# Optimization experiments

Measured on AMD Instinct MI355X. Metric: run time of the kernel, lower is better.

Reference implementation:

```python
import jax, jax.numpy as jnp
import numpy as np


def setup_inputs() -> dict:
    key = jax.random.key(0)
    k1, k2, k3 = jax.random.split(key, 3)
    B, S, E = 4, 8192, 1024
    x = jax.random.normal(k1, (B, S, E), dtype=jnp.float32)
    # torch nn.Linear weights have shape [out_features, in_features]
    W1 = jax.random.normal(k2, (3 * E, E), dtype=jnp.float32) * (1.0 / np.sqrt(E))
    W2 = jax.random.normal(k3, (E, E), dtype=jnp.float32) * (1.0 / np.sqrt(E))
    return {"x": x, "W1": W1, "W2": W2, "heads": 16}


def reference(x, W1, W2, heads):
    B, S, E = x.shape
    h = heads
    e = E // h
    # qkv projection: [B,S,3E] -> 'b s (n h e) -> n b h s e'
    qkv = (x @ W1.T).reshape(B, S, 3, h, e)
    qkv = jnp.transpose(qkv, (2, 0, 3, 1, 4))  # [3,B,h,S,e]
    q, k, v = qkv[0], qkv[1], qkv[2]
    # score: [B,h,e,e], softmax over last dim (c)
    score = jax.nn.softmax(jnp.einsum('bhnk,bhnc->bhkc', k / 4, v), axis=-1)
    # einsum 'bhnk,bhkc->bhnk': elementwise over k, sum over c
    attn = jax.nn.softmax(jnp.einsum('bhnk,bhkc->bhnk', q / 4, score), axis=-1)
    # 'b h s e -> b s (h e)' then linear_2
    out = jnp.transpose(attn, (0, 2, 1, 3)).reshape(B, S, E) @ W2.T
    return out
```

## Files before the change

kernel.cpp:

```cpp
#include <hip/hip_runtime.h>
#include <hip/hip_bf16.h>
#include <stdint.h>

static constexpr int MTOT = 32768;
static constexpr int KD   = 1024;
static constexpr int ND   = 1024;

static constexpr int BM = 128, BN = 128, BK = 64;
static constexpr int NT = KD / BK;
static constexpr int BUF_BYTES = 32768;
static constexpr int BOFF = 16384;

typedef __bf16 bf16x8 __attribute__((ext_vector_type(8)));
typedef float  f32x4  __attribute__((ext_vector_type(4)));

__device__ __forceinline__ unsigned short f2bf_rne(float f) {
  union { float f; uint32_t u; } c; c.f = f;
  uint32_t u = c.u;
  return (unsigned short)((u + 0x7fffu + ((u >> 16) & 1u)) >> 16);
}

__global__ void cast_f32_to_bf16(const float* __restrict__ src,
                                 unsigned short* __restrict__ dst, int n4) {
  int idx = blockIdx.x * blockDim.x + threadIdx.x;
  int stride = gridDim.x * blockDim.x;
  for (int i = idx; i < n4; i += stride) {
    float4 v = reinterpret_cast<const float4*>(src)[i];
    ushort4 o;
    o.x = f2bf_rne(v.x); o.y = f2bf_rne(v.y);
    o.z = f2bf_rne(v.z); o.w = f2bf_rne(v.w);
    reinterpret_cast<ushort4*>(dst)[i] = o;
  }
}

__device__ __forceinline__ void gload_lds16(const void* g, void* lds) {
  __builtin_amdgcn_global_load_lds(
      (const __attribute__((address_space(1))) unsigned int*)g,
      (__attribute__((address_space(3))) unsigned int*)lds, 16, 0, 0);
}

template <int SOFTMAX>
__global__ __launch_bounds__(256, 2)
void gemm4(const unsigned short* __restrict__ A,
           const unsigned short* __restrict__ Bm,
           void* __restrict__ Cout) {
  extern __shared__ __align__(16) char ldsc[];

  const int tid  = threadIdx.x;
  const int lane = tid & 63;
  const int wid  = tid >> 6;
  const int wm = wid >> 1, wn = wid & 1;
  const int fr = lane & 15, fq = lane >> 4;

  const int bid0 = blockIdx.x;
  const int bid  = ((bid0 & 7) << 8) | (bid0 >> 3);
  const int brow = (bid >> 3) * BM;
  const int bcol = (bid & 7) * BN;

  const int srow  = tid >> 3;
  const int sslot = (tid & 7) ^ (srow & 7);
  const unsigned short* gA = A  + (size_t)(brow + srow) * KD + sslot * 8;
  const unsigned short* gB = Bm + (size_t)(bcol + srow) * KD + sslot * 8;

  f32x4  acc[4][4] = {};
  bf16x8 a[4][2], bA[2][2], bB[2][2];

  auto STAGE = [&](const unsigned short* g, int kt, int b, int opOff) {
    #pragma unroll
    for (int i = 0; i < 4; ++i)
      gload_lds16(g + (size_t)(i * 32) * KD + kt * BK,
                  ldsc + b * BUF_BYTES + opOff + i * 4096 + tid * 16);
  };

  auto rdA = [&](int b) {
    const char* base = ldsc + b * BUF_BYTES;
    #pragma unroll
    for (int m = 0; m < 4; ++m) {
      const int r = wm * 64 + m * 16 + fr;
      #pragma unroll
      for (int ks = 0; ks < 2; ++ks)
        a[m][ks] = *(const bf16x8*)(base + (r << 7) +
                     ((ks * 64 + fq * 16) ^ ((r & 7) << 4)));
    }
  };
  auto rdB = [&](int b, int nBase, bf16x8 (*dst)[2]) {
    const char* base = ldsc + b * BUF_BYTES + BOFF;
    #pragma unroll
    for (int nn = 0; nn < 2; ++nn) {
      const int r = wn * 64 + (nBase + nn) * 16 + fr;
      #pragma unroll
      for (int ks = 0; ks < 2; ++ks)
        dst[nn][ks] = *(const bf16x8*)(base + (r << 7) +
                       ((ks * 64 + fq * 16) ^ ((r & 7) << 4)));
    }
  };
  auto MFMA16 = [&](int nBase, bf16x8 (*bf)[2]) {
    __builtin_amdgcn_s_setprio(1);
    #pragma unroll
    for (int ks = 0; ks < 2; ++ks)
      #pragma unroll
      for (int mm = 0; mm < 4; ++mm)
        #pragma unroll
        for (int nn = 0; nn < 2; ++nn)
          acc[mm][nBase + nn] = __builtin_amdgcn_mfma_f32_16x16x32_bf16(
              a[mm][ks], bf[nn][ks], acc[mm][nBase + nn], 0, 0, 0);
    __builtin_amdgcn_s_setprio(0);
  };

  auto tileStep = [&](int T, int cur, int nxt) {
    const int tp1 = (T + 1 < NT) ? T + 1 : NT - 1;
    const int tp2 = (T + 2 < NT) ? T + 2 : NT - 1;

    rdA(cur);
    STAGE(gB, tp1, nxt, BOFF);
    MFMA16(0, bA);
    __builtin_amdgcn_s_barrier();

    rdB(cur, 2, bB);
    STAGE(gA, tp2, cur, 0);
    asm volatile("s_waitcnt vmcnt(4)" ::: "memory");
    __builtin_amdgcn_s_barrier();
    rdB(nxt, 0, bA);
    MFMA16(2, bB);
    __builtin_amdgcn_s_barrier();
  };

  STAGE(gA, 0, 0, 0);
  STAGE(gB, 0, 0, BOFF);
  STAGE(gA, 1, 1, 0);
  asm volatile("s_waitcnt vmcnt(4)" ::: "memory");
  __builtin_amdgcn_s_barrier();
  rdB(0, 0, bA);

  for (int T = 0; T < NT; T += 2) {
    tileStep(T,     0, 1);
    tileStep(T + 1, 1, 0);
  }

  if constexpr (SOFTMAX) {
    unsigned short* attn = reinterpret_cast<unsigned short*>(Cout);
    constexpr float CEXP = 0.25f * 1.44269504088896340736f;
    #pragma unroll
    for (int m = 0; m < 4; ++m) {
      const int row = brow + wm * 64 + m * 16 + fq * 4;
      #pragma unroll
      for (int j = 0; j < 4; ++j) {
        float v0 = acc[m][0][j], v1 = acc[m][1][j];
        float v2 = acc[m][2][j], v3 = acc[m][3][j];
        float mx = fmaxf(fmaxf(v0, v1), fmaxf(v2, v3));
        #pragma unroll
        for (int s = 1; s < 16; s <<= 1) mx = fmaxf(mx, __shfl_xor(mx, s, 64));
        float p0 = exp2f((v0 - mx) * CEXP);
        float p1 = exp2f((v1 - mx) * CEXP);
        float p2 = exp2f((v2 - mx) * CEXP);
        float p3 = exp2f((v3 - mx) * CEXP);
        float sm = p0 + p1 + p2 + p3;
        #pragma unroll
        for (int s = 1; s < 16; s <<= 1) sm += __shfl_xor(sm, s, 64);
        const float inv = 1.0f / sm;
        unsigned short* dst =
            attn + (size_t)(row + j) * ND + (bcol + wn * 64 + fr);
        dst[0]  = f2bf_rne(p0 * inv);
        dst[16] = f2bf_rne(p1 * inv);
        dst[32] = f2bf_rne(p2 * inv);
        dst[48] = f2bf_rne(p3 * inv);
      }
    }
  } else {
    float* Cf = reinterpret_cast<float*>(Cout);
    #pragma unroll
    for (int m = 0; m < 4; ++m) {
      const int row = brow + wm * 64 + m * 16 + fq * 4;
      #pragma unroll
      for (int n = 0; n < 4; ++n) {
        const int col = bcol + wn * 64 + n * 16 + fr;
        #pragma unroll
        for (int j = 0; j < 4; ++j)
          Cf[(size_t)(row + j) * ND + col] = acc[m][n][j];
      }
    }
  }
}

extern "C" void kernel_launch(void* const* d_in, const int* in_sizes, int n_in,
                              void* d_out, int out_size, void* d_ws, size_t ws_size,
                              hipStream_t stream) {
  const float* x  = (const float*)d_in[0];
  const float* W1 = (const float*)d_in[1];
  const float* W2 = (const float*)d_in[2];
  float* out = (float*)d_out;

  char* ws = (char*)d_ws;
  unsigned short* xb   = (unsigned short*)(ws);
  unsigned short* w1b  = (unsigned short*)(ws + (size_t)67108864);
  unsigned short* w2b  = (unsigned short*)(ws + (size_t)69206016);
  unsigned short* attn = (unsigned short*)(ws + (size_t)71303168);

  hipFuncSetAttribute(reinterpret_cast<const void*>(gemm4<1>),
                      hipFuncAttributeMaxDynamicSharedMemorySize, 65536);
  hipFuncSetAttribute(reinterpret_cast<const void*>(gemm4<0>),
                      hipFuncAttributeMaxDynamicSharedMemorySize, 65536);

  cast_f32_to_bf16<<<2048, 256, 0, stream>>>(x,  xb,  MTOT * KD / 4);
  cast_f32_to_bf16<<<512,  256, 0, stream>>>(W1, w1b, KD * KD / 4);
  cast_f32_to_bf16<<<512,  256, 0, stream>>>(W2, w2b, KD * KD / 4);

  const int nblk = (MTOT / BM) * (ND / BN);
  gemm4<1><<<nblk, 256, 65536, stream>>>(xb, w1b, (void*)attn);
  gemm4<0><<<nblk, 256, 65536, stream>>>(attn, w2b, (void*)out);
}
```

Before: 195.9 us.

## Halve K tile to 32 and simplify the GEMM pipeline for higher occupancy

The K tile shrinks from 64 to 32, which halves LDS use per block to 32 KB and raises launch bounds so four blocks can share a CU instead of two. The staggered half-tile A/B schedule is replaced by a simple double buffer: each iteration reads A and B fragments, prefetches the tile two steps ahead, and issues 16 MFMAs. The LDS swizzle and global-load slot mapping are adjusted for 64-byte rows. The aim is more latency hiding through occupancy, at the cost of twice as many K iterations and barriers, less compute per barrier, and tighter register limits.

```diff
diff --git a/kernel.cpp b/kernel.cpp
--- a/kernel.cpp
+++ b/kernel.cpp
@@ -6,10 +6,10 @@
 static constexpr int KD   = 1024;
 static constexpr int ND   = 1024;
 
-static constexpr int BM = 128, BN = 128, BK = 64;
+static constexpr int BM = 128, BN = 128, BK = 32;
 static constexpr int NT = KD / BK;
-static constexpr int BUF_BYTES = 32768;
-static constexpr int BOFF = 16384;
+static constexpr int BUF_BYTES = 16384;
+static constexpr int BOFF = 8192;
 
 typedef __bf16 bf16x8 __attribute__((ext_vector_type(8)));
 typedef float  f32x4  __attribute__((ext_vector_type(4)));
@@ -40,7 +40,7 @@
 }
 
 template <int SOFTMAX>
-__global__ __launch_bounds__(256, 2)
+__global__ __launch_bounds__(256, 4)
 void gemm4(const unsigned short* __restrict__ A,
            const unsigned short* __restrict__ Bm,
            void* __restrict__ Cout) {
@@ -57,84 +57,68 @@
   const int brow = (bid >> 3) * BM;
   const int bcol = (bid & 7) * BN;
 
-  const int srow  = tid >> 3;
-  const int sslot = (tid & 7) ^ (srow & 7);
-  const unsigned short* gA = A  + (size_t)(brow + srow) * KD + sslot * 8;
-  const unsigned short* gB = Bm + (size_t)(bcol + srow) * KD + sslot * 8;
+  const int srow  = tid >> 2;
+  const int gslot = (tid & 3) ^ ((tid >> 3) & 3);
+  const unsigned short* gA = A  + (size_t)(brow + srow) * KD + gslot * 8;
+  const unsigned short* gB = Bm + (size_t)(bcol + srow) * KD + gslot * 8;
 
   f32x4  acc[4][4] = {};
-  bf16x8 a[4][2], bA[2][2], bB[2][2];
+  bf16x8 a[4], b[4];
 
-  auto STAGE = [&](const unsigned short* g, int kt, int b, int opOff) {
+  auto STAGE = [&](const unsigned short* g, int kt, int bfp, int opOff) {
     #pragma unroll
-    for (int i = 0; i < 4; ++i)
-      gload_lds16(g + (size_t)(i * 32) * KD + kt * BK,
-                  ldsc + b * BUF_BYTES + opOff + i * 4096 + tid * 16);
+    for (int i = 0; i < 2; ++i)
+      gload_lds16(g + (size_t)(i * 64) * KD + kt * BK,
+                  ldsc + bfp * BUF_BYTES + opOff + i * 4096 + tid * 16);
   };
 
-  auto rdA = [&](int b) {
-    const char* base = ldsc + b * BUF_BYTES;
+  auto rdA = [&](int bfp) {
+    const char* base = ldsc + bfp * BUF_BYTES;
     #pragma unroll
     for (int m = 0; m < 4; ++m) {
       const int r = wm * 64 + m * 16 + fr;
-      #pragma unroll
-      for (int ks = 0; ks < 2; ++ks)
-        a[m][ks] = *(const bf16x8*)(base + (r << 7) +
-                     ((ks * 64 + fq * 16) ^ ((r & 7) << 4)));
+      a[m] = *(const bf16x8*)(base + (r << 6) +
+                              ((fq << 4) ^ (((r >> 1) & 3) << 4)));
     }
   };
-  auto rdB = [&](int b, int nBase, bf16x8 (*dst)[2]) {
-    const char* base = ldsc + b * BUF_BYTES + BOFF;
+  auto rdB = [&](int bfp) {
+    const char* base = ldsc + bfp * BUF_BYTES + BOFF;
     #pragma unroll
-    for (int nn = 0; nn < 2; ++nn) {
-      const int r = wn * 64 + (nBase + nn) * 16 + fr;
-      #pragma unroll
-      for (int ks = 0; ks < 2; ++ks)
-        dst[nn][ks] = *(const bf16x8*)(base + (r << 7) +
-                       ((ks * 64 + fq * 16) ^ ((r & 7) << 4)));
+    for (int n = 0; n < 4; ++n) {
+      const int r = wn * 64 + n * 16 + fr;
+      b[n] = *(const bf16x8*)(base + (r << 6) +
+                              ((fq << 4) ^ (((r >> 1) & 3) << 4)));
     }
   };
-  auto MFMA16 = [&](int nBase, bf16x8 (*bf)[2]) {
+
+  STAGE(gA, 0, 0, 0); STAGE(gB, 0, 0, BOFF);
+  STAGE(gA, 1, 1, 0); STAGE(gB, 1, 1, BOFF);
+  asm volatile("s_waitcnt vmcnt(4)" ::: "memory");
+  __builtin_amdgcn_s_barrier();
+
+  #pragma unroll 2
+  for (int T = 0; T < NT; ++T) {
+    const int cur = T & 1;
+    const int tp2 = (T + 2 < NT) ? T + 2 : NT - 1;
+
+    rdA(cur); rdB(cur);
+    asm volatile("s_waitcnt lgkmcnt(0)" ::: "memory");
+    __builtin_amdgcn_s_barrier();
+
+    STAGE(gA, tp2, cur, 0);
+    STAGE(gB, tp2, cur, BOFF);
+
     __builtin_amdgcn_s_setprio(1);
     #pragma unroll
-    for (int ks = 0; ks < 2; ++ks)
+    for (int m = 0; m < 4; ++m)
       #pragma unroll
-      for (int mm = 0; mm < 4; ++mm)
-        #pragma unroll
-        for (int nn = 0; nn < 2; ++nn)
-          acc[mm][nBase + nn] = __builtin_amdgcn_mfma_f32_16x16x32_bf16(
-              a[mm][ks], bf[nn][ks], acc[mm][nBase + nn], 0, 0, 0);
+      for (int n = 0; n < 4; ++n)
+        acc[m][n] = __builtin_amdgcn_mfma_f32_16x16x32_bf16(
+            a[m], b[n], acc[m][n], 0, 0, 0);
     __builtin_amdgcn_s_setprio(0);
-  };
 
-  auto tileStep = [&](int T, int cur, int nxt) {
-    const int tp1 = (T + 1 < NT) ? T + 1 : NT - 1;
-    const int tp2 = (T + 2 < NT) ? T + 2 : NT - 1;
-
-    rdA(cur);
-    STAGE(gB, tp1, nxt, BOFF);
-    MFMA16(0, bA);
-    __builtin_amdgcn_s_barrier();
-
-    rdB(cur, 2, bB);
-    STAGE(gA, tp2, cur, 0);
     asm volatile("s_waitcnt vmcnt(4)" ::: "memory");
     __builtin_amdgcn_s_barrier();
-    rdB(nxt, 0, bA);
-    MFMA16(2, bB);
-    __builtin_amdgcn_s_barrier();
-  };
-
-  STAGE(gA, 0, 0, 0);
-  STAGE(gB, 0, 0, BOFF);
-  STAGE(gA, 1, 1, 0);
-  asm volatile("s_waitcnt vmcnt(4)" ::: "memory");
-  __builtin_amdgcn_s_barrier();
-  rdB(0, 0, bA);
-
-  for (int T = 0; T < NT; T += 2) {
-    tileStep(T,     0, 1);
-    tileStep(T + 1, 1, 0);
   }
 
   if constexpr (SOFTMAX) {
@@ -197,15 +181,15 @@
   unsigned short* attn = (unsigned short*)(ws + (size_t)71303168);
 
   hipFuncSetAttribute(reinterpret_cast<const void*>(gemm4<1>),
-                      hipFuncAttributeMaxDynamicSharedMemorySize, 65536);
+                      hipFuncAttributeMaxDynamicSharedMemorySize, 32768);
   hipFuncSetAttribute(reinterpret_cast<const void*>(gemm4<0>),
-                      hipFuncAttributeMaxDynamicSharedMemorySize, 65536);
+                      hipFuncAttributeMaxDynamicSharedMemorySize, 32768);
 
   cast_f32_to_bf16<<<2048, 256, 0, stream>>>(x,  xb,  MTOT * KD / 4);
   cast_f32_to_bf16<<<512,  256, 0, stream>>>(W1, w1b, KD * KD / 4);
   cast_f32_to_bf16<<<512,  256, 0, stream>>>(W2, w2b, KD * KD / 4);
 
   const int nblk = (MTOT / BM) * (ND / BN);
-  gemm4<1><<<nblk, 256, 65536, stream>>>(xb, w1b, (void*)attn);
-  gemm4<0><<<nblk, 256, 65536, stream>>>(attn, w2b, (void*)out);
+  gemm4<1><<<nblk, 256, 32768, stream>>>(xb, w1b, (void*)attn);
+  gemm4<0><<<nblk, 256, 32768, stream>>>(attn, w2b, (void*)out);
 }
```

New measurement: 218.6 us. 11.6% more time.
